# Kernel optimization log

Measured on AMD Instinct MI355X. Metric: run time of the kernel, lower is better.

## Reference

```python
import jax, jax.numpy as jnp
import numpy as np

V = 49152      # HEALPix nside=64 pixel count
B = 2
FIN = 32
FOUT = 64
K = 8          # Chebyshev kernel_size
DEG = 8        # neighbors per pixel (plus self-loop -> 9 nnz/row)
G = 8          # GroupNorm num_groups
EPS = 1e-5
SLOPE = 0.1    # LeakyReLU negative slope


def setup_inputs() -> dict:
    key = jax.random.key(0)
    ks = jax.random.split(key, 4)
    rng = np.random.default_rng(0)
    # sparse Laplacian in COO: 8 random neighbors + self-loop per node
    row = np.repeat(np.arange(V, dtype=np.int32), DEG + 1)
    nbrs = rng.integers(0, V, size=(V, DEG))
    col = np.concatenate([nbrs, np.arange(V)[:, None]], axis=1).astype(np.int32).reshape(-1)
    vals = (rng.standard_normal(V * (DEG + 1)).astype(np.float32)) * 0.1
    x = jax.random.normal(ks[0], (B, V, FIN), dtype=jnp.float32)
    W1 = jax.random.normal(ks[1], (K, FIN, FOUT), dtype=jnp.float32) * 0.05
    W2 = jax.random.normal(ks[2], (K, FOUT, FOUT), dtype=jnp.float32) * 0.05
    Wr = jax.random.normal(ks[3], (K, FIN, FOUT), dtype=jnp.float32) * 0.05
    zeros = jnp.zeros((FOUT,), dtype=jnp.float32)
    ones = jnp.ones((FOUT,), dtype=jnp.float32)
    return {
        "x": x,
        "lap_vals": jnp.asarray(vals),
        "lap_row": jnp.asarray(row),
        "lap_col": jnp.asarray(col),
        "W1": W1, "b1": zeros, "g1": ones, "be1": zeros,
        "W2": W2, "b2": zeros, "g2": ones, "be2": zeros,
        "Wr": Wr, "br": zeros,
    }


def _spmm(vals, row, col, z):
    # L @ z for COO Laplacian; z: [V, D]
    return jax.ops.segment_sum(vals[:, None] * z[col], row, num_segments=V)


def _cheb_conv(x, vals, row, col, W, b):
    # x: [B, V, Fin], W: [K, Fin, Fout] -> [B, V, Fout]
    Bb, Vv, F = x.shape
    x0 = jnp.transpose(x, (1, 0, 2)).reshape(Vv, Bb * F)  # [V, B*F]
    xs = [x0, _spmm(vals, row, col, x0)]
    for _ in range(K - 2):
        xs.append(2.0 * _spmm(vals, row, col, xs[-1]) - xs[-2])
    Xk = jnp.stack(xs, 0).reshape(K, Vv, Bb, F)
    Xk = jnp.transpose(Xk, (2, 1, 0, 3))  # [B, V, K, F]
    return jnp.einsum('bvkf,kfo->bvo', Xk, W) + b


def _group_norm(x, gamma, beta):
    # equivalent to nn.GroupNorm applied on x.permute(0,2,1): normalize over (C/G, V)
    Bb, Vv, C = x.shape
    xg = x.reshape(Bb, Vv, G, C // G)
    mu = xg.mean(axis=(1, 3), keepdims=True)
    var = xg.var(axis=(1, 3), keepdims=True)
    xn = ((xg - mu) * jax.lax.rsqrt(var + EPS)).reshape(Bb, Vv, C)
    return xn * gamma + beta


def _block(x, vals, row, col, W, b, gamma, beta):
    h = _cheb_conv(x, vals, row, col, W, b)
    h = _group_norm(h, gamma, beta)
    return jax.nn.leaky_relu(h, SLOPE)  # out_channels > 1 -> LeakyReLU(0.1)


def reference(x, lap_vals, lap_row, lap_col, W1, b1, g1, be1, W2, b2, g2, be2, Wr, br):
    h = _block(x, lap_vals, lap_row, lap_col, W1, b1, g1, be1)
    h = _block(h, lap_vals, lap_row, lap_col, W2, b2, g2, be2)
    res = _cheb_conv(x, lap_vals, lap_row, lap_col, Wr, br)  # in != out -> res_conv
    return h + res
```

## Files before the change

kernel.cpp:

```cpp
#include <hip/hip_runtime.h>
#include <hip/hip_bf16.h>

#define V 49152
#define NNZ 9
#define EPSV 1e-5f
#define SLOPE 0.1f

typedef __attribute__((ext_vector_type(8))) short bf16x8;
typedef __attribute__((ext_vector_type(4))) float f32x4;

__device__ __forceinline__ float lo2f(unsigned u) { return __uint_as_float(u << 16); }
__device__ __forceinline__ float hi2f(unsigned u) { return __uint_as_float(u & 0xffff0000u); }
__device__ __forceinline__ unsigned short f2us(float f) {
    __hip_bfloat16 h = __float2bfloat16(f);
    return *(unsigned short*)&h;
}
__device__ __forceinline__ float us2f(unsigned short u) { return __uint_as_float(((unsigned)u) << 16); }
__device__ __forceinline__ unsigned pk2(float a, float b) {
    return ((unsigned)f2us(a)) | (((unsigned)f2us(b)) << 16);
}

__device__ __forceinline__ void gload_lds16(const void* g, void* l) {
    __builtin_amdgcn_global_load_lds((__attribute__((address_space(1))) void*)g,
                                     (__attribute__((address_space(3))) void*)l, 16, 0, 0);
}

__global__ __launch_bounds__(256) void prep_k(
    const float* __restrict__ W1, const float* __restrict__ Wr, const float* __restrict__ W2,
    unsigned short* __restrict__ Wt1, unsigned short* __restrict__ Wtr, unsigned short* __restrict__ Wt2,
    float* __restrict__ part)
{
    int i = blockIdx.x * 256 + threadIdx.x;
    if (i < 32768) {
        int kk = i >> 12, rem = i & 4095, o = rem >> 6, f = rem & 63;
        Wt2[i] = f2us(W2[kk * 4096 + f * 64 + o]);
    } else if (i < 49152) {
        int j = i - 32768;
        int kk = j >> 11, rem = j & 2047, o = rem >> 5, f = rem & 31;
        Wt1[j] = f2us(W1[kk * 2048 + f * 64 + o]);
    } else if (i < 65536) {
        int j = i - 49152;
        int kk = j >> 11, rem = j & 2047, o = rem >> 5, f = rem & 31;
        Wtr[j] = f2us(Wr[kk * 2048 + f * 64 + o]);
    } else if (i < 66560) {
        part[i - 65536] = 0.f;
    }
}

__global__ __launch_bounds__(256) void reorder_k(const float* __restrict__ x, unsigned* __restrict__ t0) {
    int idx = blockIdx.x * 256 + threadIdx.x;
    int v = idx >> 5, j2 = idx & 31;
    int b = j2 >> 4, f0 = (j2 & 15) * 2;
    const float* p = x + ((size_t)b * V + v) * 32 + f0;
    t0[idx] = pk2(p[0], p[1]);
}

template<int THR, bool FIRST>
__global__ __launch_bounds__(256) void spmm_step(
    const uint4* __restrict__ zc, const uint4* __restrict__ zp, uint4* __restrict__ zn,
    const float* __restrict__ vals, const int* __restrict__ col)
{
    constexpr int L4 = THR * 2;
    int tid = blockIdx.x * 256 + threadIdx.x;
    int v = tid / THR;
    int c = (tid - v * THR) * 2;
    int base = v * NNZ;
    float t[16];
    #pragma unroll
    for (int i = 0; i < 16; ++i) t[i] = 0.f;
    #pragma unroll
    for (int n = 0; n < NNZ; ++n) {
        float a = vals[base + n];
        int cc = col[base + n];
        const uint4* p = zc + (size_t)cc * L4 + c;
        uint4 u0 = p[0];
        uint4 u1 = p[1];
        t[0] += a * lo2f(u0.x); t[1] += a * hi2f(u0.x);
        t[2] += a * lo2f(u0.y); t[3] += a * hi2f(u0.y);
        t[4] += a * lo2f(u0.z); t[5] += a * hi2f(u0.z);
        t[6] += a * lo2f(u0.w); t[7] += a * hi2f(u0.w);
        t[8]  += a * lo2f(u1.x); t[9]  += a * hi2f(u1.x);
        t[10] += a * lo2f(u1.y); t[11] += a * hi2f(u1.y);
        t[12] += a * lo2f(u1.z); t[13] += a * hi2f(u1.z);
        t[14] += a * lo2f(u1.w); t[15] += a * hi2f(u1.w);
    }
    if (!FIRST) {
        const uint4* pp = zp + (size_t)v * L4 + c;
        uint4 p0 = pp[0];
        uint4 p1 = pp[1];
        t[0] = 2.f*t[0] - lo2f(p0.x); t[1] = 2.f*t[1] - hi2f(p0.x);
        t[2] = 2.f*t[2] - lo2f(p0.y); t[3] = 2.f*t[3] - hi2f(p0.y);
        t[4] = 2.f*t[4] - lo2f(p0.z); t[5] = 2.f*t[5] - hi2f(p0.z);
        t[6] = 2.f*t[6] - lo2f(p0.w); t[7] = 2.f*t[7] - hi2f(p0.w);
        t[8]  = 2.f*t[8]  - lo2f(p1.x); t[9]  = 2.f*t[9]  - hi2f(p1.x);
        t[10] = 2.f*t[10] - lo2f(p1.y); t[11] = 2.f*t[11] - hi2f(p1.y);
        t[12] = 2.f*t[12] - lo2f(p1.z); t[13] = 2.f*t[13] - hi2f(p1.z);
        t[14] = 2.f*t[14] - lo2f(p1.w); t[15] = 2.f*t[15] - hi2f(p1.w);
    }
    uint4 r0, r1;
    r0.x = pk2(t[0], t[1]);  r0.y = pk2(t[2], t[3]);
    r0.z = pk2(t[4], t[5]);  r0.w = pk2(t[6], t[7]);
    r1.x = pk2(t[8], t[9]);  r1.y = pk2(t[10], t[11]);
    r1.z = pk2(t[12], t[13]); r1.w = pk2(t[14], t[15]);
    uint4* q = zn + (size_t)v * L4 + c;
    q[0] = r0;
    q[1] = r1;
}

template<int F, int NKK, int NPH, bool DUAL, bool INIT, bool FINAL>
__global__ __launch_bounds__(256) void mfma_gemm(
    const unsigned short* __restrict__ T,
    const unsigned short* __restrict__ WtA, const unsigned short* __restrict__ WtB,
    const float* __restrict__ biasA, const float* __restrict__ biasB,
    unsigned short* __restrict__ ACC, float* __restrict__ resOut,
    float* __restrict__ part)
{
    constexpr int KPP = NKK / NPH;
    constexpr int CPR = F / 4;
    constexpr int FH = F / 32;
    constexpr int RST = 68;
    constexpr int STAGE_SH = KPP * 64 * 2 * F;
    constexpr int TRANS_SH = (DUAL ? 2 : 1) * 2 * 64 * RST * 2;
    constexpr int SH = STAGE_SH > TRANS_SH ? STAGE_SH : TRANS_SH;
    __shared__ unsigned short shraw[SH];
    __shared__ float sGrp[32];

    unsigned short* tile = shraw;
    float* accbuf  = (float*)shraw;
    float* dualbuf = accbuf + 2 * 64 * RST;

    int wv = threadIdx.x >> 6, lane = threadIdx.x & 63;
    int quad = lane >> 4, l15 = lane & 15;
    int v0 = blockIdx.x * 64;
    int ot = wv;

    bf16x8 bw[NKK][FH];
    bf16x8 bd[NKK][FH];
    f32x4 acc[4][2];
    f32x4 accd[4][2];

    #pragma unroll
    for (int ph = 0; ph < NPH; ++ph) {
        if (ph > 0) __syncthreads();

        #pragma unroll
        for (int i = 0; i < (KPP * 64 * CPR) / 256; ++i) {
            int s = (i * 4 + wv) * 64 + lane;
            int kkl = s / (64 * CPR);
            int ws = s - kkl * 64 * CPR;
            int row = ws / CPR;
            int cl = ws - row * CPR;
            int cg = (cl & ~7) | ((cl & 7) ^ (row & 7));
            const unsigned short* gp =
                T + ((size_t)(ph * KPP + kkl) * V + v0 + row) * (2 * F) + cg * 8;
            gload_lds16(gp, tile + (size_t)(i * 4 + wv) * 64 * 8);
        }

        if (ph == 0) {
            #pragma unroll
            for (int kk = 0; kk < NKK; ++kk) {
                #pragma unroll
                for (int fh = 0; fh < FH; ++fh) {
                    size_t brow = ((size_t)kk * 64 + ot * 16 + l15) * F + fh * 32 + quad * 8;
                    bw[kk][fh] = *(const bf16x8*)(const void*)(WtA + brow);
                    if constexpr (DUAL) bd[kk][fh] = *(const bf16x8*)(const void*)(WtB + brow);
                }
            }
            #pragma unroll
            for (int m = 0; m < 4; ++m)
                #pragma unroll
                for (int b = 0; b < 2; ++b) {
                    acc[m][b] = (f32x4){0.f, 0.f, 0.f, 0.f};
                    if constexpr (DUAL) accd[m][b] = (f32x4){0.f, 0.f, 0.f, 0.f};
                }
        }

        __syncthreads();

        #pragma unroll
        for (int kkl = 0; kkl < KPP; ++kkl) {
            int kk = ph * KPP + kkl;
            #pragma unroll
            for (int fh = 0; fh < FH; ++fh) {
                #pragma unroll
                for (int m = 0; m < 4; ++m) {
                    int r = m * 16 + l15;
                    int rx = r & 7;
                    const unsigned short* rbase = tile + ((size_t)kkl * 64 + r) * 2 * F;
                    #pragma unroll
                    for (int b = 0; b < 2; ++b) {
                        int c0 = b * (CPR / 2) + fh * 4 + quad;
                        int s0 = (c0 & ~7) | ((c0 & 7) ^ rx);
                        bf16x8 a = *(const bf16x8*)(const void*)(rbase + s0 * 8);
                        acc[m][b] = __builtin_amdgcn_mfma_f32_16x16x32_bf16(a, bw[kk][fh], acc[m][b], 0, 0, 0);
                        if constexpr (DUAL)
                            accd[m][b] = __builtin_amdgcn_mfma_f32_16x16x32_bf16(a, bd[kk][fh], accd[m][b], 0, 0, 0);
                    }
                }
            }
        }
    }

    __syncthreads();

    int o = ot * 16 + l15;
    float bia = FINAL ? biasA[o] : 0.f;
    float biaB = DUAL ? biasB[o] : 0.f;
    #pragma unroll
    for (int m = 0; m < 4; ++m) {
        #pragma unroll
        for (int b = 0; b < 2; ++b) {
            #pragma unroll
            for (int rr = 0; rr < 4; ++rr) {
                int r = m * 16 + quad * 4 + rr;
                accbuf[(b * 64 + r) * RST + o] = acc[m][b][rr] + bia;
                if constexpr (DUAL) dualbuf[(b * 64 + r) * RST + o] = accd[m][b][rr] + biaB;
            }
        }
    }
    if constexpr (FINAL) {
        if (threadIdx.x < 32) sGrp[threadIdx.x] = 0.f;
    }
    __syncthreads();

    #pragma unroll
    for (int j = 0; j < 4; ++j) {
        int cid = threadIdx.x + 256 * j;
        int g = cid & 7, r = (cid >> 3) & 63, b = cid >> 9;
        int o0 = g * 8;
        const float* src = accbuf + (b * 64 + r) * RST + o0;
        float e[8];
        #pragma unroll
        for (int i = 0; i < 8; ++i) e[i] = src[i];
        size_t gidx = ((size_t)b * V + v0 + r) * 64 + o0;
        if constexpr (!INIT) {
            uint4 old = *(const uint4*)(const void*)(ACC + gidx);
            e[0] += lo2f(old.x); e[1] += hi2f(old.x);
            e[2] += lo2f(old.y); e[3] += hi2f(old.y);
            e[4] += lo2f(old.z); e[5] += hi2f(old.z);
            e[6] += lo2f(old.w); e[7] += hi2f(old.w);
        }
        uint4 pk;
        pk.x = pk2(e[0], e[1]); pk.y = pk2(e[2], e[3]);
        pk.z = pk2(e[4], e[5]); pk.w = pk2(e[6], e[7]);
        *(uint4*)(void*)(ACC + gidx) = pk;
        if constexpr (FINAL) {
            float s = 0.f, q = 0.f;
            #pragma unroll
            for (int i = 0; i < 8; ++i) { s += e[i]; q += e[i] * e[i]; }
            atomicAdd(&sGrp[b * 8 + g], s);
            atomicAdd(&sGrp[16 + b * 8 + g], q);
        }
    }
    if constexpr (DUAL) {
        #pragma unroll
        for (int j = 0; j < 8; ++j) {
            int cid = threadIdx.x + 256 * j;
            int oc = cid & 15, r = (cid >> 4) & 63, b = cid >> 10;
            float4 vv = *(const float4*)(const void*)(dualbuf + (b * 64 + r) * RST + oc * 4);
            *(float4*)(void*)(resOut + ((size_t)b * V + v0 + r) * 64 + oc * 4) = vv;
        }
    }
    if constexpr (FINAL) {
        __syncthreads();
        if (threadIdx.x < 16) {
            atomicAdd(&part[threadIdx.x * 2],     sGrp[threadIdx.x]);
            atomicAdd(&part[threadIdx.x * 2 + 1], sGrp[16 + threadIdx.x]);
        }
    }
}

__global__ __launch_bounds__(256) void gn_apply(const unsigned short* __restrict__ ACC,
                                                const float* __restrict__ part,
                                                const float* __restrict__ gamma, const float* __restrict__ beta,
                                                unsigned* __restrict__ zout) {
    int idx = blockIdx.x * 256 + threadIdx.x;
    int v = idx >> 4, j = idx & 15;
    int b = j >> 3, g = j & 7;
    const float N = (float)V * 8.f;
    float mean = part[j * 2] / N;
    float rstd = rsqrtf(part[j * 2 + 1] / N - mean * mean + EPSV);
    int o0 = g * 8;
    uint4 aa = *(const uint4*)(const void*)(ACC + ((size_t)b * V + v) * 64 + o0);
    float e[8] = { lo2f(aa.x), hi2f(aa.x), lo2f(aa.y), hi2f(aa.y),
                   lo2f(aa.z), hi2f(aa.z), lo2f(aa.w), hi2f(aa.w) };
    float y[8];
    #pragma unroll
    for (int i = 0; i < 8; ++i) {
        float t = (e[i] - mean) * rstd * gamma[o0 + i] + beta[o0 + i];
        y[i] = t > 0.f ? t : SLOPE * t;
    }
    uint4 pk;
    pk.x = pk2(y[0], y[1]); pk.y = pk2(y[2], y[3]);
    pk.z = pk2(y[4], y[5]); pk.w = pk2(y[6], y[7]);
    *(uint4*)(void*)(zout + (size_t)v * 64 + b * 32 + g * 4) = pk;
}

__global__ __launch_bounds__(256) void final_out(const unsigned short* __restrict__ ACC,
                                                 float* outres,
                                                 const float* __restrict__ part,
                                                 const float* __restrict__ gamma, const float* __restrict__ beta) {
    int idx = blockIdx.x * 256 + threadIdx.x;
    int b = idx >= V * 8 ? 1 : 0;
    int r = idx - b * V * 8;
    int v = r >> 3, g = r & 7;
    int j = b * 8 + g;
    const float N = (float)V * 8.f;
    float mean = part[j * 2] / N;
    float rstd = rsqrtf(part[j * 2 + 1] / N - mean * mean + EPSV);
    int o0 = g * 8;
    size_t base = ((size_t)b * V + v) * 64 + o0;
    uint4 aa = *(const uint4*)(const void*)(ACC + base);
    float e[8] = { lo2f(aa.x), hi2f(aa.x), lo2f(aa.y), hi2f(aa.y),
                   lo2f(aa.z), hi2f(aa.z), lo2f(aa.w), hi2f(aa.w) };
    float4 r0 = *(const float4*)(const void*)(outres + base);
    float4 r1 = *(const float4*)(const void*)(outres + base + 4);
    float y[8];
    #pragma unroll
    for (int i = 0; i < 8; ++i) {
        float t = (e[i] - mean) * rstd * gamma[o0 + i] + beta[o0 + i];
        y[i] = t > 0.f ? t : SLOPE * t;
    }
    float4 w0 = { y[0] + r0.x, y[1] + r0.y, y[2] + r0.z, y[3] + r0.w };
    float4 w1 = { y[4] + r1.x, y[5] + r1.y, y[6] + r1.z, y[7] + r1.w };
    *(float4*)(void*)(outres + base) = w0;
    *(float4*)(void*)(outres + base + 4) = w1;
}

extern "C" void kernel_launch(void* const* d_in, const int* in_sizes, int n_in,
                              void* d_out, int out_size, void* d_ws, size_t ws_size,
                              hipStream_t stream) {
    const float* x    = (const float*)d_in[0];
    const float* vals = (const float*)d_in[1];
    const int*   col  = (const int*)d_in[3];
    const float* W1   = (const float*)d_in[4];
    const float* b1   = (const float*)d_in[5];
    const float* g1   = (const float*)d_in[6];
    const float* be1  = (const float*)d_in[7];
    const float* W2   = (const float*)d_in[8];
    const float* b2   = (const float*)d_in[9];
    const float* g2   = (const float*)d_in[10];
    const float* be2  = (const float*)d_in[11];
    const float* Wr   = (const float*)d_in[12];
    const float* br   = (const float*)d_in[13];
    float* out = (float*)d_out;

    unsigned short* TS  = (unsigned short*)d_ws;
    unsigned short* ACC = TS + (size_t)8 * V * 128;
    unsigned short* Wt1 = ACC + (size_t)2 * V * 64;
    unsigned short* Wtr = Wt1 + 8 * 64 * 32;
    unsigned short* Wt2 = Wtr + 8 * 64 * 32;
    float* PART1 = (float*)(Wt2 + 8 * 64 * 64);
    float* PART2 = PART1 + 32;

    prep_k<<<260, 256, 0, stream>>>(W1, Wr, W2, Wt1, Wtr, Wt2, PART1);

    uint4* T1s[8];
    for (int k = 0; k < 8; ++k) T1s[k] = (uint4*)(TS + (size_t)k * V * 64);

    reorder_k<<<V * 32 / 256, 256, 0, stream>>>(x, (unsigned*)T1s[0]);
    spmm_step<4, true><<<V * 4 / 256, 256, 0, stream>>>(T1s[0], nullptr, T1s[1], vals, col);
    for (int k = 2; k < 8; ++k)
        spmm_step<4, false><<<V * 4 / 256, 256, 0, stream>>>(T1s[k-1], T1s[k-2], T1s[k], vals, col);

    mfma_gemm<32, 8, 1, true, true, true><<<V / 64, 256, 0, stream>>>(
        TS, Wt1, Wtr, b1, br, ACC, out, PART1);

    uint4* T2s[8];
    for (int k = 0; k < 8; ++k) T2s[k] = (uint4*)(TS + (size_t)k * V * 128);

    gn_apply<<<V * 16 / 256, 256, 0, stream>>>(ACC, PART1, g1, be1, (unsigned*)T2s[0]);
    spmm_step<8, true><<<V * 8 / 256, 256, 0, stream>>>(T2s[0], nullptr, T2s[1], vals, col);
    for (int k = 2; k < 8; ++k)
        spmm_step<8, false><<<V * 8 / 256, 256, 0, stream>>>(T2s[k-1], T2s[k-2], T2s[k], vals, col);

    mfma_gemm<64, 8, 2, false, true, true><<<V / 64, 256, 0, stream>>>(
        TS, Wt2, nullptr, b2, nullptr, ACC, nullptr, PART2);

    final_out<<<2 * V * 8 / 256, 256, 0, stream>>>(ACC, out, PART2, g2, be2);
}
```

Before: 364.7 us.

## Fuse last Chebyshev SpMM and GroupNorm apply into GEMMs, merge prep kernels

Merges weight prep and the input reorder into a single launch. The last SpMM step of each Chebyshev chain now runs inside the GEMM kernel and writes straight into the LDS tile, so T7 is never written to or read from global memory. GroupNorm+LeakyReLU of block 1 is folded into the first two SpMM steps and the second GEMM, which recompute it on the fly instead of materializing T0. The cost is redundant GN recomputation and per-block gather latency inside the GEMMs, which may lower their occupancy.

```diff
diff --git a/kernel.cpp b/kernel.cpp
--- a/kernel.cpp
+++ b/kernel.cpp
@@ -5,6 +5,7 @@
 #define NNZ 9
 #define EPSV 1e-5f
 #define SLOPE 0.1f
+#define RST 68
 
 typedef __attribute__((ext_vector_type(8))) short bf16x8;
 typedef __attribute__((ext_vector_type(4))) float f32x4;
@@ -15,44 +16,71 @@
     __hip_bfloat16 h = __float2bfloat16(f);
     return *(unsigned short*)&h;
 }
-__device__ __forceinline__ float us2f(unsigned short u) { return __uint_as_float(((unsigned)u) << 16); }
 __device__ __forceinline__ unsigned pk2(float a, float b) {
     return ((unsigned)f2us(a)) | (((unsigned)f2us(b)) << 16);
 }
-
+__device__ __forceinline__ void fma8(float* t, float a, uint4 u) {
+    t[0] += a * lo2f(u.x); t[1] += a * hi2f(u.x);
+    t[2] += a * lo2f(u.y); t[3] += a * hi2f(u.y);
+    t[4] += a * lo2f(u.z); t[5] += a * hi2f(u.z);
+    t[6] += a * lo2f(u.w); t[7] += a * hi2f(u.w);
+}
+__device__ __forceinline__ void fold8(float* t, uint4 p) {
+    t[0] = 2.f*t[0] - lo2f(p.x); t[1] = 2.f*t[1] - hi2f(p.x);
+    t[2] = 2.f*t[2] - lo2f(p.y); t[3] = 2.f*t[3] - hi2f(p.y);
+    t[4] = 2.f*t[4] - lo2f(p.z); t[5] = 2.f*t[5] - hi2f(p.z);
+    t[6] = 2.f*t[6] - lo2f(p.w); t[7] = 2.f*t[7] - hi2f(p.w);
+}
+__device__ __forceinline__ uint4 pack8(const float* t) {
+    uint4 r;
+    r.x = pk2(t[0], t[1]); r.y = pk2(t[2], t[3]);
+    r.z = pk2(t[4], t[5]); r.w = pk2(t[6], t[7]);
+    return r;
+}
+__device__ __forceinline__ void gnleaky8(uint4 u, const float* scl, const float* sft, float* y) {
+    float e[8] = { lo2f(u.x), hi2f(u.x), lo2f(u.y), hi2f(u.y),
+                   lo2f(u.z), hi2f(u.z), lo2f(u.w), hi2f(u.w) };
+    #pragma unroll
+    for (int i = 0; i < 8; ++i) {
+        float t = e[i] * scl[i] + sft[i];
+        y[i] = t > 0.f ? t : SLOPE * t;
+    }
+}
 __device__ __forceinline__ void gload_lds16(const void* g, void* l) {
     __builtin_amdgcn_global_load_lds((__attribute__((address_space(1))) void*)g,
                                      (__attribute__((address_space(3))) void*)l, 16, 0, 0);
 }
 
-__global__ __launch_bounds__(256) void prep_k(
+__global__ __launch_bounds__(256) void prep_reorder_k(
+    const float* __restrict__ x, unsigned* __restrict__ t0,
     const float* __restrict__ W1, const float* __restrict__ Wr, const float* __restrict__ W2,
     unsigned short* __restrict__ Wt1, unsigned short* __restrict__ Wtr, unsigned short* __restrict__ Wt2,
     float* __restrict__ part)
 {
-    int i = blockIdx.x * 256 + threadIdx.x;
-    if (i < 32768) {
-        int kk = i >> 12, rem = i & 4095, o = rem >> 6, f = rem & 63;
-        Wt2[i] = f2us(W2[kk * 4096 + f * 64 + o]);
-    } else if (i < 49152) {
-        int j = i - 32768;
-        int kk = j >> 11, rem = j & 2047, o = rem >> 5, f = rem & 31;
-        Wt1[j] = f2us(W1[kk * 2048 + f * 64 + o]);
-    } else if (i < 65536) {
-        int j = i - 49152;
-        int kk = j >> 11, rem = j & 2047, o = rem >> 5, f = rem & 31;
-        Wtr[j] = f2us(Wr[kk * 2048 + f * 64 + o]);
-    } else if (i < 66560) {
-        part[i - 65536] = 0.f;
-    }
-}
-
-__global__ __launch_bounds__(256) void reorder_k(const float* __restrict__ x, unsigned* __restrict__ t0) {
-    int idx = blockIdx.x * 256 + threadIdx.x;
-    int v = idx >> 5, j2 = idx & 31;
-    int b = j2 >> 4, f0 = (j2 & 15) * 2;
-    const float* p = x + ((size_t)b * V + v) * 32 + f0;
-    t0[idx] = pk2(p[0], p[1]);
+    int bid = blockIdx.x;
+    if (bid < 6144) {
+        int idx = bid * 256 + threadIdx.x;
+        int v = idx >> 5, j2 = idx & 31;
+        int b = j2 >> 4, f0 = (j2 & 15) * 2;
+        const float* p = x + ((size_t)b * V + v) * 32 + f0;
+        t0[idx] = pk2(p[0], p[1]);
+    } else {
+        int i = (bid - 6144) * 256 + threadIdx.x;
+        if (i < 32768) {
+            int kk = i >> 12, rem = i & 4095, o = rem >> 6, f = rem & 63;
+            Wt2[i] = f2us(W2[kk * 4096 + f * 64 + o]);
+        } else if (i < 49152) {
+            int j = i - 32768;
+            int kk = j >> 11, rem = j & 2047, o = rem >> 5, f = rem & 31;
+            Wt1[j] = f2us(W1[kk * 2048 + f * 64 + o]);
+        } else if (i < 65536) {
+            int j = i - 49152;
+            int kk = j >> 11, rem = j & 2047, o = rem >> 5, f = rem & 31;
+            Wtr[j] = f2us(Wr[kk * 2048 + f * 64 + o]);
+        } else if (i < 66560) {
+            part[i - 65536] = 0.f;
+        }
+    }
 }
 
 template<int THR, bool FIRST>
@@ -73,58 +101,92 @@
         float a = vals[base + n];
         int cc = col[base + n];
         const uint4* p = zc + (size_t)cc * L4 + c;
-        uint4 u0 = p[0];
-        uint4 u1 = p[1];
-        t[0] += a * lo2f(u0.x); t[1] += a * hi2f(u0.x);
-        t[2] += a * lo2f(u0.y); t[3] += a * hi2f(u0.y);
-        t[4] += a * lo2f(u0.z); t[5] += a * hi2f(u0.z);
-        t[6] += a * lo2f(u0.w); t[7] += a * hi2f(u0.w);
-        t[8]  += a * lo2f(u1.x); t[9]  += a * hi2f(u1.x);
-        t[10] += a * lo2f(u1.y); t[11] += a * hi2f(u1.y);
-        t[12] += a * lo2f(u1.z); t[13] += a * hi2f(u1.z);
-        t[14] += a * lo2f(u1.w); t[15] += a * hi2f(u1.w);
+        fma8(t, a, p[0]);
+        fma8(t + 8, a, p[1]);
     }
     if (!FIRST) {
         const uint4* pp = zp + (size_t)v * L4 + c;
-        uint4 p0 = pp[0];
-        uint4 p1 = pp[1];
-        t[0] = 2.f*t[0] - lo2f(p0.x); t[1] = 2.f*t[1] - hi2f(p0.x);
-        t[2] = 2.f*t[2] - lo2f(p0.y); t[3] = 2.f*t[3] - hi2f(p0.y);
-        t[4] = 2.f*t[4] - lo2f(p0.z); t[5] = 2.f*t[5] - hi2f(p0.z);
-        t[6] = 2.f*t[6] - lo2f(p0.w); t[7] = 2.f*t[7] - hi2f(p0.w);
-        t[8]  = 2.f*t[8]  - lo2f(p1.x); t[9]  = 2.f*t[9]  - hi2f(p1.x);
-        t[10] = 2.f*t[10] - lo2f(p1.y); t[11] = 2.f*t[11] - hi2f(p1.y);
-        t[12] = 2.f*t[12] - lo2f(p1.z); t[13] = 2.f*t[13] - hi2f(p1.z);
-        t[14] = 2.f*t[14] - lo2f(p1.w); t[15] = 2.f*t[15] - hi2f(p1.w);
-    }
-    uint4 r0, r1;
-    r0.x = pk2(t[0], t[1]);  r0.y = pk2(t[2], t[3]);
-    r0.z = pk2(t[4], t[5]);  r0.w = pk2(t[6], t[7]);
-    r1.x = pk2(t[8], t[9]);  r1.y = pk2(t[10], t[11]);
-    r1.z = pk2(t[12], t[13]); r1.w = pk2(t[14], t[15]);
+        fold8(t, pp[0]);
+        fold8(t + 8, pp[1]);
+    }
     uint4* q = zn + (size_t)v * L4 + c;
-    q[0] = r0;
-    q[1] = r1;
-}
-
-template<int F, int NKK, int NPH, bool DUAL, bool INIT, bool FINAL>
-__global__ __launch_bounds__(256) void mfma_gemm(
+    q[0] = pack8(t);
+    q[1] = pack8(t + 8);
+}
+
+template<int MODE>
+__global__ __launch_bounds__(256) void spmm2_gn(
+    const unsigned short* __restrict__ ACC, const uint4* __restrict__ zc,
+    uint4* __restrict__ zn, const float* __restrict__ part,
+    const float* __restrict__ gamma, const float* __restrict__ beta,
+    const float* __restrict__ vals, const int* __restrict__ col)
+{
+    int tid = blockIdx.x * 256 + threadIdx.x;
+    int v = tid >> 3;
+    int c2 = (tid & 7) * 2;
+    int b = c2 >> 3;
+    int ch0 = (c2 & 7) * 8;
+    const float Nf = (float)V * 8.f;
+    int g0 = c2 & 7;
+    float m0 = part[(b*8+g0)*2] / Nf;
+    float r0 = rsqrtf(part[(b*8+g0)*2+1]/Nf - m0*m0 + EPSV);
+    float m1 = part[(b*8+g0+1)*2] / Nf;
+    float r1 = rsqrtf(part[(b*8+g0+1)*2+1]/Nf - m1*m1 + EPSV);
+    float scl[16], sft[16];
+    #pragma unroll
+    for (int i = 0; i < 8; ++i) {
+        int o = ch0 + i;
+        scl[i] = r0 * gamma[o];     sft[i] = beta[o] - m0 * scl[i];
+        scl[8+i] = r1 * gamma[o+8]; sft[8+i] = beta[o+8] - m1 * scl[8+i];
+    }
+
+    float t[16];
+    #pragma unroll
+    for (int i = 0; i < 16; ++i) t[i] = 0.f;
+    int base = v * NNZ;
+    #pragma unroll
+    for (int n = 0; n < NNZ; ++n) {
+        float a = vals[base + n];
+        int cc = col[base + n];
+        if constexpr (MODE == 0) {
+            const uint4* p = (const uint4*)(const void*)(ACC + ((size_t)b * V + cc) * 64 + ch0);
+            float y[8];
+            gnleaky8(p[0], scl, sft, y);
+            #pragma unroll
+            for (int i = 0; i < 8; ++i) t[i] += a * y[i];
+            gnleaky8(p[1], scl + 8, sft + 8, y);
+            #pragma unroll
+            for (int i = 0; i < 8; ++i) t[8 + i] += a * y[i];
+        } else {
+            const uint4* p = zc + (size_t)cc * 16 + c2;
+            fma8(t, a, p[0]);
+            fma8(t + 8, a, p[1]);
+        }
+    }
+    if constexpr (MODE == 1) {
+        const uint4* pp = (const uint4*)(const void*)(ACC + ((size_t)b * V + v) * 64 + ch0);
+        float y[8];
+        gnleaky8(pp[0], scl, sft, y);
+        #pragma unroll
+        for (int i = 0; i < 8; ++i) t[i] = 2.f * t[i] - y[i];
+        gnleaky8(pp[1], scl + 8, sft + 8, y);
+        #pragma unroll
+        for (int i = 0; i < 8; ++i) t[8 + i] = 2.f * t[8 + i] - y[i];
+    }
+    uint4* q = zn + (size_t)v * 16 + c2;
+    q[0] = pack8(t);
+    q[1] = pack8(t + 8);
+}
+
+__global__ __launch_bounds__(256) void gemm1f(
     const unsigned short* __restrict__ T,
     const unsigned short* __restrict__ WtA, const unsigned short* __restrict__ WtB,
     const float* __restrict__ biasA, const float* __restrict__ biasB,
-    unsigned short* __restrict__ ACC, float* __restrict__ resOut,
-    float* __restrict__ part)
+    const float* __restrict__ vals, const int* __restrict__ col,
+    unsigned short* __restrict__ ACC, float* __restrict__ resOut, float* __restrict__ part)
 {
-    constexpr int KPP = NKK / NPH;
-    constexpr int CPR = F / 4;
-    constexpr int FH = F / 32;
-    constexpr int RST = 68;
-    constexpr int STAGE_SH = KPP * 64 * 2 * F;
-    constexpr int TRANS_SH = (DUAL ? 2 : 1) * 2 * 64 * RST * 2;
-    constexpr int SH = STAGE_SH > TRANS_SH ? STAGE_SH : TRANS_SH;
-    __shared__ unsigned short shraw[SH];
+    __shared__ unsigned short shraw[34816];
     __shared__ float sGrp[32];
-
     unsigned short* tile = shraw;
     float* accbuf  = (float*)shraw;
     float* dualbuf = accbuf + 2 * 64 * RST;
@@ -134,166 +196,300 @@
     int v0 = blockIdx.x * 64;
     int ot = wv;
 
-    bf16x8 bw[NKK][FH];
-    bf16x8 bd[NKK][FH];
-    f32x4 acc[4][2];
-    f32x4 accd[4][2];
-
-    #pragma unroll
-    for (int ph = 0; ph < NPH; ++ph) {
-        if (ph > 0) __syncthreads();
-
-        #pragma unroll
-        for (int i = 0; i < (KPP * 64 * CPR) / 256; ++i) {
-            int s = (i * 4 + wv) * 64 + lane;
-            int kkl = s / (64 * CPR);
-            int ws = s - kkl * 64 * CPR;
-            int row = ws / CPR;
-            int cl = ws - row * CPR;
-            int cg = (cl & ~7) | ((cl & 7) ^ (row & 7));
-            const unsigned short* gp =
-                T + ((size_t)(ph * KPP + kkl) * V + v0 + row) * (2 * F) + cg * 8;
-            gload_lds16(gp, tile + (size_t)(i * 4 + wv) * 64 * 8);
-        }
-
-        if (ph == 0) {
-            #pragma unroll
-            for (int kk = 0; kk < NKK; ++kk) {
-                #pragma unroll
-                for (int fh = 0; fh < FH; ++fh) {
-                    size_t brow = ((size_t)kk * 64 + ot * 16 + l15) * F + fh * 32 + quad * 8;
-                    bw[kk][fh] = *(const bf16x8*)(const void*)(WtA + brow);
-                    if constexpr (DUAL) bd[kk][fh] = *(const bf16x8*)(const void*)(WtB + brow);
-                }
+    #pragma unroll
+    for (int i = 0; i < 14; ++i) {
+        int s = (i * 4 + wv) * 64 + lane;
+        int kkl = s >> 9;
+        int ws = s & 511;
+        int row = ws >> 3;
+        int cl = ws & 7;
+        int cg = cl ^ (row & 7);
+        const unsigned short* gp = T + ((size_t)kkl * V + v0 + row) * 64 + cg * 8;
+        gload_lds16(gp, tile + (size_t)(i * 4 + wv) * 64 * 8);
+    }
+
+    {
+        const unsigned short* T6 = T + (size_t)6 * V * 64;
+        const unsigned short* T5 = T + (size_t)5 * V * 64;
+        int row = threadIdx.x >> 2, c2 = (threadIdx.x & 3) * 2;
+        int gv = v0 + row;
+        float t[16];
+        #pragma unroll
+        for (int i = 0; i < 16; ++i) t[i] = 0.f;
+        int base = gv * NNZ;
+        #pragma unroll
+        for (int n = 0; n < NNZ; ++n) {
+            float a = vals[base + n];
+            int cc = col[base + n];
+            const uint4* p = (const uint4*)(const void*)(T6 + (size_t)cc * 64 + c2 * 8);
+            fma8(t, a, p[0]);
+            fma8(t + 8, a, p[1]);
+        }
+        const uint4* pp = (const uint4*)(const void*)(T5 + (size_t)gv * 64 + c2 * 8);
+        fold8(t, pp[0]);
+        fold8(t + 8, pp[1]);
+        uint4* tl = (uint4*)tile;
+        int r7 = row & 7;
+        tl[(7 * 64 + row) * 8 + (c2 ^ r7)]       = pack8(t);
+        tl[(7 * 64 + row) * 8 + ((c2 + 1) ^ r7)] = pack8(t + 8);
+    }
+
+    bf16x8 bw[8], bd[8];
+    #pragma unroll
+    for (int kk = 0; kk < 8; ++kk) {
+        size_t brow = ((size_t)kk * 64 + ot * 16 + l15) * 32 + quad * 8;
+        bw[kk] = *(const bf16x8*)(const void*)(WtA + brow);
+        bd[kk] = *(const bf16x8*)(const void*)(WtB + brow);
+    }
+    f32x4 acc[4][2], accd[4][2];
+    #pragma unroll
+    for (int m = 0; m < 4; ++m)
+        #pragma unroll
+        for (int b = 0; b < 2; ++b) {
+            acc[m][b]  = (f32x4){0.f, 0.f, 0.f, 0.f};
+            accd[m][b] = (f32x4){0.f, 0.f, 0.f, 0.f};
+        }
+    __syncthreads();
+
+    #pragma unroll
+    for (int kk = 0; kk < 8; ++kk) {
+        #pragma unroll
+        for (int m = 0; m < 4; ++m) {
+            int r = m * 16 + l15;
+            int rx = r & 7;
+            const unsigned short* rbase = tile + ((size_t)kk * 64 + r) * 64;
+            #pragma unroll
+            for (int b = 0; b < 2; ++b) {
+                int s0 = (b * 4 + quad) ^ rx;
+                bf16x8 a = *(const bf16x8*)(const void*)(rbase + s0 * 8);
+                acc[m][b]  = __builtin_amdgcn_mfma_f32_16x16x32_bf16(a, bw[kk], acc[m][b], 0, 0, 0);
+                accd[m][b] = __builtin_amdgcn_mfma_f32_16x16x32_bf16(a, bd[kk], accd[m][b], 0, 0, 0);
             }
-            #pragma unroll
-            for (int m = 0; m < 4; ++m)
-                #pragma unroll
-                for (int b = 0; b < 2; ++b) {
-                    acc[m][b] = (f32x4){0.f, 0.f, 0.f, 0.f};
-                    if constexpr (DUAL) accd[m][b] = (f32x4){0.f, 0.f, 0.f, 0.f};
-                }
-        }
-
-        __syncthreads();
-
-        #pragma unroll
-        for (int kkl = 0; kkl < KPP; ++kkl) {
-            int kk = ph * KPP + kkl;
-            #pragma unroll
-            for (int fh = 0; fh < FH; ++fh) {
-                #pragma unroll
-                for (int m = 0; m < 4; ++m) {
-                    int r = m * 16 + l15;
-                    int rx = r & 7;
-                    const unsigned short* rbase = tile + ((size_t)kkl * 64 + r) * 2 * F;
-                    #pragma unroll
-                    for (int b = 0; b < 2; ++b) {
-                        int c0 = b * (CPR / 2) + fh * 4 + quad;
-                        int s0 = (c0 & ~7) | ((c0 & 7) ^ rx);
-                        bf16x8 a = *(const bf16x8*)(const void*)(rbase + s0 * 8);
-                        acc[m][b] = __builtin_amdgcn_mfma_f32_16x16x32_bf16(a, bw[kk][fh], acc[m][b], 0, 0, 0);
-                        if constexpr (DUAL)
-                            accd[m][b] = __builtin_amdgcn_mfma_f32_16x16x32_bf16(a, bd[kk][fh], accd[m][b], 0, 0, 0);
-                    }
-                }
-            }
-        }
-    }
-
-    __syncthreads();
-
+        }
+    }
+
+    __syncthreads();
     int o = ot * 16 + l15;
-    float bia = FINAL ? biasA[o] : 0.f;
-    float biaB = DUAL ? biasB[o] : 0.f;
-    #pragma unroll
-    for (int m = 0; m < 4; ++m) {
-        #pragma unroll
-        for (int b = 0; b < 2; ++b) {
+    float biA = biasA[o], biB = biasB[o];
+    #pragma unroll
+    for (int m = 0; m < 4; ++m)
+        #pragma unroll
+        for (int b = 0; b < 2; ++b)
             #pragma unroll
             for (int rr = 0; rr < 4; ++rr) {
                 int r = m * 16 + quad * 4 + rr;
-                accbuf[(b * 64 + r) * RST + o] = acc[m][b][rr] + bia;
-                if constexpr (DUAL) dualbuf[(b * 64 + r) * RST + o] = accd[m][b][rr] + biaB;
+                accbuf[(b * 64 + r) * RST + o] = acc[m][b][rr] + biA;
+                dualbuf[(b * 64 + r) * RST + o] = accd[m][b][rr] + biB;
             }
-        }
-    }
-    if constexpr (FINAL) {
-        if (threadIdx.x < 32) sGrp[threadIdx.x] = 0.f;
-    }
-    __syncthreads();
-
+    if (threadIdx.x < 32) sGrp[threadIdx.x] = 0.f;
+    __syncthreads();
     #pragma unroll
     for (int j = 0; j < 4; ++j) {
         int cid = threadIdx.x + 256 * j;
         int g = cid & 7, r = (cid >> 3) & 63, b = cid >> 9;
+        const float* src = accbuf + (b * 64 + r) * RST + g * 8;
+        float e[8], s = 0.f, q = 0.f;
+        #pragma unroll
+        for (int i = 0; i < 8; ++i) { e[i] = src[i]; s += e[i]; q += e[i] * e[i]; }
+        *(uint4*)(void*)(ACC + ((size_t)b * V + v0 + r) * 64 + g * 8) = pack8(e);
+        atomicAdd(&sGrp[b * 8 + g], s);
+        atomicAdd(&sGrp[16 + b * 8 + g], q);
+    }
+    #pragma unroll
+    for (int j = 0; j < 8; ++j) {
+        int cid = threadIdx.x + 256 * j;
+        int oc = cid & 15, r = (cid >> 4) & 63, b = cid >> 10;
+        float4 vv = *(const float4*)(const void*)(dualbuf + (b * 64 + r) * RST + oc * 4);
+        *(float4*)(void*)(resOut + ((size_t)b * V + v0 + r) * 64 + oc * 4) = vv;
+    }
+    __syncthreads();
+    if (threadIdx.x < 16) {
+        atomicAdd(&part[threadIdx.x * 2],     sGrp[threadIdx.x]);
+        atomicAdd(&part[threadIdx.x * 2 + 1], sGrp[16 + threadIdx.x]);
+    }
+}
+
+__global__ __launch_bounds__(256) void gemm2f(
+    const unsigned short* __restrict__ T,
+    unsigned short* ACC,
+    const float* __restrict__ part1, const float* __restrict__ g1, const float* __restrict__ be1,
+    const unsigned short* __restrict__ Wt2, const float* __restrict__ biasA,
+    float* __restrict__ part2,
+    const float* __restrict__ vals, const int* __restrict__ col)
+{
+    __shared__ unsigned short shraw[32768];
+    __shared__ float sGrp[32];
+    unsigned short* tile = shraw;
+    float* accbuf = (float*)shraw;
+
+    int wv = threadIdx.x >> 6, lane = threadIdx.x & 63;
+    int quad = lane >> 4, l15 = lane & 15;
+    int v0 = blockIdx.x * 64;
+    int ot = wv;
+    const float Nf = (float)V * 8.f;
+
+    #pragma unroll
+    for (int i = 4; i < 16; ++i) {
+        int s = (i * 4 + wv) * 64 + lane;
+        int kkl = s >> 10;
+        int ws = s & 1023;
+        int row = ws >> 4;
+        int cl = ws & 15;
+        int cg = (cl & ~7) | ((cl & 7) ^ (row & 7));
+        const unsigned short* gp = T + ((size_t)kkl * V + v0 + row) * 128 + cg * 8;
+        gload_lds16(gp, tile + (size_t)(i * 4 + wv) * 64 * 8);
+    }
+    {
+        int cl = threadIdx.x & 15;
+        int b = cl >> 3, g = cl & 7, j8 = b * 8 + g;
+        float mean = part1[j8 * 2] / Nf;
+        float rstd = rsqrtf(part1[j8 * 2 + 1] / Nf - mean * mean + EPSV);
         int o0 = g * 8;
-        const float* src = accbuf + (b * 64 + r) * RST + o0;
-        float e[8];
-        #pragma unroll
-        for (int i = 0; i < 8; ++i) e[i] = src[i];
-        size_t gidx = ((size_t)b * V + v0 + r) * 64 + o0;
-        if constexpr (!INIT) {
-            uint4 old = *(const uint4*)(const void*)(ACC + gidx);
-            e[0] += lo2f(old.x); e[1] += hi2f(old.x);
-            e[2] += lo2f(old.y); e[3] += hi2f(old.y);
-            e[4] += lo2f(old.z); e[5] += hi2f(old.z);
-            e[6] += lo2f(old.w); e[7] += hi2f(old.w);
-        }
-        uint4 pk;
-        pk.x = pk2(e[0], e[1]); pk.y = pk2(e[2], e[3]);
-        pk.z = pk2(e[4], e[5]); pk.w = pk2(e[6], e[7]);
-        *(uint4*)(void*)(ACC + gidx) = pk;
-        if constexpr (FINAL) {
-            float s = 0.f, q = 0.f;
-            #pragma unroll
-            for (int i = 0; i < 8; ++i) { s += e[i]; q += e[i] * e[i]; }
-            atomicAdd(&sGrp[b * 8 + g], s);
-            atomicAdd(&sGrp[16 + b * 8 + g], q);
-        }
-    }
-    if constexpr (DUAL) {
-        #pragma unroll
-        for (int j = 0; j < 8; ++j) {
-            int cid = threadIdx.x + 256 * j;
-            int oc = cid & 15, r = (cid >> 4) & 63, b = cid >> 10;
-            float4 vv = *(const float4*)(const void*)(dualbuf + (b * 64 + r) * RST + oc * 4);
-            *(float4*)(void*)(resOut + ((size_t)b * V + v0 + r) * 64 + oc * 4) = vv;
-        }
-    }
-    if constexpr (FINAL) {
-        __syncthreads();
-        if (threadIdx.x < 16) {
-            atomicAdd(&part[threadIdx.x * 2],     sGrp[threadIdx.x]);
-            atomicAdd(&part[threadIdx.x * 2 + 1], sGrp[16 + threadIdx.x]);
-        }
-    }
-}
-
-__global__ __launch_bounds__(256) void gn_apply(const unsigned short* __restrict__ ACC,
-                                                const float* __restrict__ part,
-                                                const float* __restrict__ gamma, const float* __restrict__ beta,
-                                                unsigned* __restrict__ zout) {
-    int idx = blockIdx.x * 256 + threadIdx.x;
-    int v = idx >> 4, j = idx & 15;
-    int b = j >> 3, g = j & 7;
-    const float N = (float)V * 8.f;
-    float mean = part[j * 2] / N;
-    float rstd = rsqrtf(part[j * 2 + 1] / N - mean * mean + EPSV);
-    int o0 = g * 8;
-    uint4 aa = *(const uint4*)(const void*)(ACC + ((size_t)b * V + v) * 64 + o0);
-    float e[8] = { lo2f(aa.x), hi2f(aa.x), lo2f(aa.y), hi2f(aa.y),
-                   lo2f(aa.z), hi2f(aa.z), lo2f(aa.w), hi2f(aa.w) };
-    float y[8];
-    #pragma unroll
-    for (int i = 0; i < 8; ++i) {
-        float t = (e[i] - mean) * rstd * gamma[o0 + i] + beta[o0 + i];
-        y[i] = t > 0.f ? t : SLOPE * t;
-    }
-    uint4 pk;
-    pk.x = pk2(y[0], y[1]); pk.y = pk2(y[2], y[3]);
-    pk.z = pk2(y[4], y[5]); pk.w = pk2(y[6], y[7]);
-    *(uint4*)(void*)(zout + (size_t)v * 64 + b * 32 + g * 4) = pk;
+        float scl[8], sft[8];
+        #pragma unroll
+        for (int i = 0; i < 8; ++i) {
+            scl[i] = rstd * g1[o0 + i];
+            sft[i] = be1[o0 + i] - mean * scl[i];
+        }
+        uint4* tl = (uint4*)tile;
+        #pragma unroll
+        for (int j = 0; j < 4; ++j) {
+            int r = (threadIdx.x >> 4) + 16 * j;
+            uint4 aa = *(const uint4*)(const void*)(ACC + ((size_t)b * V + v0 + r) * 64 + o0);
+            float y[8];
+            gnleaky8(aa, scl, sft, y);
+            tl[r * 16 + ((cl & ~7) | ((cl & 7) ^ (r & 7)))] = pack8(y);
+        }
+    }
+    bf16x8 bw[8][2];
+    #pragma unroll
+    for (int kk = 0; kk < 8; ++kk)
+        #pragma unroll
+        for (int fh = 0; fh < 2; ++fh) {
+            size_t brow = ((size_t)kk * 64 + ot * 16 + l15) * 64 + fh * 32 + quad * 8;
+            bw[kk][fh] = *(const bf16x8*)(const void*)(Wt2 + brow);
+        }
+    f32x4 acc[4][2];
+    #pragma unroll
+    for (int m = 0; m < 4; ++m)
+        #pragma unroll
+        for (int b = 0; b < 2; ++b) acc[m][b] = (f32x4){0.f, 0.f, 0.f, 0.f};
+    __syncthreads();
+
+    #pragma unroll
+    for (int kkl = 0; kkl < 4; ++kkl) {
+        #pragma unroll
+        for (int m = 0; m < 4; ++m) {
+            int r = m * 16 + l15, rx = r & 7;
+            const unsigned short* rbase = tile + ((size_t)kkl * 64 + r) * 128;
+            #pragma unroll
+            for (int b = 0; b < 2; ++b)
+                #pragma unroll
+                for (int fh = 0; fh < 2; ++fh) {
+                    int c0 = b * 8 + fh * 4 + quad;
+                    int s0 = (c0 & ~7) | ((c0 & 7) ^ rx);
+                    bf16x8 a = *(const bf16x8*)(const void*)(rbase + s0 * 8);
+                    acc[m][b] = __builtin_amdgcn_mfma_f32_16x16x32_bf16(a, bw[kkl][fh], acc[m][b], 0, 0, 0);
+                }
+        }
+    }
+    __syncthreads();
+
+    #pragma unroll
+    for (int i = 0; i < 12; ++i) {
+        int s = (i * 4 + wv) * 64 + lane;
+        int kkl = s >> 10;
+        int ws = s & 1023;
+        int row = ws >> 4;
+        int cl = ws & 15;
+        int cg = (cl & ~7) | ((cl & 7) ^ (row & 7));
+        const unsigned short* gp = T + ((size_t)(4 + kkl) * V + v0 + row) * 128 + cg * 8;
+        gload_lds16(gp, tile + (size_t)(i * 4 + wv) * 64 * 8);
+    }
+    {
+        const unsigned short* T6 = T + (size_t)6 * V * 128;
+        const unsigned short* T5 = T + (size_t)5 * V * 128;
+        int row = threadIdx.x >> 2, cb = (threadIdx.x & 3) * 4;
+        int gv = v0 + row;
+        float t[32];
+        #pragma unroll
+        for (int i = 0; i < 32; ++i) t[i] = 0.f;
+        int base = gv * NNZ;
+        #pragma unroll
+        for (int n = 0; n < NNZ; ++n) {
+            float a = vals[base + n];
+            int cc = col[base + n];
+            const uint4* p = (const uint4*)(const void*)(T6 + (size_t)cc * 128 + cb * 8);
+            fma8(t, a, p[0]);
+            fma8(t + 8, a, p[1]);
+            fma8(t + 16, a, p[2]);
+            fma8(t + 24, a, p[3]);
+        }
+        const uint4* pp = (const uint4*)(const void*)(T5 + (size_t)gv * 128 + cb * 8);
+        fold8(t, pp[0]);
+        fold8(t + 8, pp[1]);
+        fold8(t + 16, pp[2]);
+        fold8(t + 24, pp[3]);
+        uint4* tl = (uint4*)tile;
+        int r7 = row & 7;
+        #pragma unroll
+        for (int q = 0; q < 4; ++q) {
+            int c = cb + q;
+            tl[(3 * 64 + row) * 16 + ((c & ~7) | ((c & 7) ^ r7))] = pack8(t + q * 8);
+        }
+    }
+    __syncthreads();
+
+    #pragma unroll
+    for (int kkl = 0; kkl < 4; ++kkl) {
+        int kk = 4 + kkl;
+        #pragma unroll
+        for (int m = 0; m < 4; ++m) {
+            int r = m * 16 + l15, rx = r & 7;
+            const unsigned short* rbase = tile + ((size_t)kkl * 64 + r) * 128;
+            #pragma unroll
+            for (int b = 0; b < 2; ++b)
+                #pragma unroll
+                for (int fh = 0; fh < 2; ++fh) {
+                    int c0 = b * 8 + fh * 4 + quad;
+                    int s0 = (c0 & ~7) | ((c0 & 7) ^ rx);
+                    bf16x8 a = *(const bf16x8*)(const void*)(rbase + s0 * 8);
+                    acc[m][b] = __builtin_amdgcn_mfma_f32_16x16x32_bf16(a, bw[kk][fh], acc[m][b], 0, 0, 0);
+                }
+        }
+    }
+
+    __syncthreads();
+    int o = ot * 16 + l15;
+    float biA = biasA[o];
+    #pragma unroll
+    for (int m = 0; m < 4; ++m)
+        #pragma unroll
+        for (int b = 0; b < 2; ++b)
+            #pragma unroll
+            for (int rr = 0; rr < 4; ++rr) {
+                int r = m * 16 + quad * 4 + rr;
+                accbuf[(b * 64 + r) * RST + o] = acc[m][b][rr] + biA;
+            }
+    if (threadIdx.x < 32) sGrp[threadIdx.x] = 0.f;
+    __syncthreads();
+    #pragma unroll
+    for (int j = 0; j < 4; ++j) {
+        int cid = threadIdx.x + 256 * j;
+        int g = cid & 7, r = (cid >> 3) & 63, b = cid >> 9;
+        const float* src = accbuf + (b * 64 + r) * RST + g * 8;
+        float e[8], s = 0.f, q = 0.f;
+        #pragma unroll
+        for (int i = 0; i < 8; ++i) { e[i] = src[i]; s += e[i]; q += e[i] * e[i]; }
+        *(uint4*)(void*)(ACC + ((size_t)b * V + v0 + r) * 64 + g * 8) = pack8(e);
+        atomicAdd(&sGrp[b * 8 + g], s);
+        atomicAdd(&sGrp[16 + b * 8 + g], q);
+    }
+    __syncthreads();
+    if (threadIdx.x < 16) {
+        atomicAdd(&part2[threadIdx.x * 2],     sGrp[threadIdx.x]);
+        atomicAdd(&part2[threadIdx.x * 2 + 1], sGrp[16 + threadIdx.x]);
+    }
 }
 
 __global__ __launch_bounds__(256) void final_out(const unsigned short* __restrict__ ACC,
@@ -353,29 +549,24 @@
     float* PART1 = (float*)(Wt2 + 8 * 64 * 64);
     float* PART2 = PART1 + 32;
 
-    prep_k<<<260, 256, 0, stream>>>(W1, Wr, W2, Wt1, Wtr, Wt2, PART1);
+    prep_reorder_k<<<6404, 256, 0, stream>>>(x, (unsigned*)TS, W1, Wr, W2, Wt1, Wtr, Wt2, PART1);
 
     uint4* T1s[8];
     for (int k = 0; k < 8; ++k) T1s[k] = (uint4*)(TS + (size_t)k * V * 64);
-
-    reorder_k<<<V * 32 / 256, 256, 0, stream>>>(x, (unsigned*)T1s[0]);
     spmm_step<4, true><<<V * 4 / 256, 256, 0, stream>>>(T1s[0], nullptr, T1s[1], vals, col);
-    for (int k = 2; k < 8; ++k)
+    for (int k = 2; k < 7; ++k)
         spmm_step<4, false><<<V * 4 / 256, 256, 0, stream>>>(T1s[k-1], T1s[k-2], T1s[k], vals, col);
 
-    mfma_gemm<32, 8, 1, true, true, true><<<V / 64, 256, 0, stream>>>(
-        TS, Wt1, Wtr, b1, br, ACC, out, PART1);
+    gemm1f<<<V / 64, 256, 0, stream>>>(TS, Wt1, Wtr, b1, br, vals, col, ACC, out, PART1);
 
     uint4* T2s[8];
     for (int k = 0; k < 8; ++k) T2s[k] = (uint4*)(TS + (size_t)k * V * 128);
-
-    gn_apply<<<V * 16 / 256, 256, 0, stream>>>(ACC, PART1, g1, be1, (unsigned*)T2s[0]);
-    spmm_step<8, true><<<V * 8 / 256, 256, 0, stream>>>(T2s[0], nullptr, T2s[1], vals, col);
-    for (int k = 2; k < 8; ++k)
+    spmm2_gn<0><<<V * 8 / 256, 256, 0, stream>>>(ACC, nullptr, T2s[1], PART1, g1, be1, vals, col);
+    spmm2_gn<1><<<V * 8 / 256, 256, 0, stream>>>(ACC, T2s[1], T2s[2], PART1, g1, be1, vals, col);
+    for (int k = 3; k < 7; ++k)
         spmm_step<8, false><<<V * 8 / 256, 256, 0, stream>>>(T2s[k-1], T2s[k-2], T2s[k], vals, col);
 
-    mfma_gemm<64, 8, 2, false, true, true><<<V / 64, 256, 0, stream>>>(
-        TS, Wt2, nullptr, b2, nullptr, ACC, nullptr, PART2);
+    gemm2f<<<V / 64, 256, 0, stream>>>(TS, ACC, PART1, g1, be1, Wt2, b2, PART2, vals, col);
 
     final_out<<<2 * V * 8 / 256, 256, 0, stream>>>(ACC, out, PART2, g2, be2);
 }
```

After: 364.1 us. No clear change (-0.2%).
